# Kernel optimization log

Hardware: AMD Instinct MI355X
Metric: run time of the kernel (lower is better)

The kernel has to match this reference:

```python
import jax, jax.numpy as jnp
import numpy as np

PI = float(np.pi)
N_DIST, N_THETA = 4, 8   # projection_dict
MAX_DIST = 0.2           # self.max_dist (estimated from nh distances in __init__)


def _distance_angle(lon1, lat1, lon2, lat2):
    # great-circle distance + bearing ('polar' base of get_distance_angle)
    dlon = lon2 - lon1
    cos_d = jnp.sin(lat1) * jnp.sin(lat2) + jnp.cos(lat1) * jnp.cos(lat2) * jnp.cos(dlon)
    d = jnp.arccos(jnp.clip(cos_d, -1.0 + 1e-7, 1.0 - 1e-7))
    phi = jnp.arctan2(jnp.sin(dlon) * jnp.cos(lat2),
                      jnp.cos(lat1) * jnp.sin(lat2) - jnp.sin(lat1) * jnp.cos(lat2) * jnp.cos(dlon))
    return d, phi


def _forward(x, coordinates, sigma_d, kappa_vm, local_indices, adjc):
    # x: [B,N,E]; adjc: [Ncells,NH]; coordinates: [2,Ncells]; local_indices: [B,N]
    sigma_d = jnp.reshape(sigma_d, ())
    kappa_vm = jnp.reshape(kappa_vm, ())
    indices_nh = adjc[local_indices]                              # [B,N,NH] (get_nh_indices)
    # gather_nh_data (sample offsets are zero: sampled_level == global_level, sample==0)
    x_nh = jax.vmap(lambda xb, ib: xb[ib])(x, indices_nh)         # [B,N,NH,E]
    coords_nh = coordinates[:, indices_nh]                        # [2,B,N,NH]
    # get_relative_positions(coords_nh[:,:,:,0], coords_nh, polar=True):
    # coords1 -> [2,B,N,1,1], coords2 -> [2,B,N,1,NH]  => dists/phis [B,N,1,NH]
    lon_c = coords_nh[0, :, :, 0][..., None, None]                # [B,N,1,1]
    lat_c = coords_nh[1, :, :, 0][..., None, None]
    lon_nh = coords_nh[0][:, :, None, :]                          # [B,N,1,NH]
    lat_nh = coords_nh[1][:, :, None, :]
    dists, phis = _distance_angle(lon_c, lat_c, lon_nh, lat_nh)   # [B,N,1,NH]
    thetas_proj = jnp.linspace(-PI, PI, N_THETA + 1)[:-1]         # [T]
    dists_proj = jnp.linspace(0.0, MAX_DIST, N_DIST)              # [D]
    # von_mises: [D?,T,1] - [B,N,1,1,NH] broadcast -> we keep factored forms
    vm = jnp.exp(kappa_vm * jnp.cos(thetas_proj[None, :, None] - phis[..., None, :]))        # [B,N,1,T,NH]
    nd = jnp.exp(-0.5 * ((dists_proj[:, None, None] - dists[..., None, :]) / sigma_d) ** 2)  # [B,N,D,1,NH]
    w = vm * nd                                                   # [B,N,D,T,NH]
    w = w / (w.sum(axis=-1, keepdims=True) + 1e-10)
    # proj_data: weighted sum over neighborhood -> [B,N,D,T,E]
    return jnp.einsum('bndtk,bnke->bndte', w, x_nh)


def setup_inputs() -> dict:
    key = jax.random.key(0)
    k1, k2, k3 = jax.random.split(key, 3)
    B, N, NH, E = 1, 65536, 7, 16
    x = jax.random.normal(k1, (B, N, E), dtype=jnp.float32)
    # lon/lat in a small local patch (radians) so neighbor distances are O(MAX_DIST)
    coordinates = jax.random.uniform(k2, (2, N), dtype=jnp.float32) * 0.2
    adjc = jax.random.randint(k3, (N, NH), 0, N, dtype=jnp.int32)
    local_indices = jnp.arange(N, dtype=jnp.int32)[None, :]       # [B,N]
    sigma_d = jnp.full((1,), 0.05, dtype=jnp.float32)
    kappa_vm = jnp.full((1,), 2.0, dtype=jnp.float32)
    return {"x": x, "coordinates": coordinates, "sigma_d": sigma_d,
            "kappa_vm": kappa_vm, "local_indices": local_indices, "adjc": adjc}


def reference(x, coordinates, sigma_d, kappa_vm, local_indices, adjc):
    return _forward(x, coordinates, sigma_d, kappa_vm, local_indices, adjc)
```

## Files before the change

kernel.cpp:

```cpp
#include <hip/hip_runtime.h>
#include <math.h>

constexpr int NH     = 7;
constexpr int NDIST  = 4;
constexpr int NTHETA = 8;
constexpr int EDIM   = 16;
constexpr int NPB    = 8;
constexpr int BLOCK  = 256;

typedef float f32x4 __attribute__((ext_vector_type(4)));

__global__ __launch_bounds__(BLOCK) void grid_layer_kernel(
    const float* __restrict__ x,
    const float* __restrict__ coords,
    const float* __restrict__ sigma_p,
    const float* __restrict__ kappa_p,
    const int*   __restrict__ lidx,
    const int*   __restrict__ adjc,
    float*       __restrict__ out,
    int N)
{
    __shared__ float4 xs[NPB][NH][EDIM / 4];
    __shared__ float4 vm4[NPB][NH][2];
    __shared__ float4 nd4[NPB][NH];
    __shared__ float4 ctr[NPB];
    __shared__ int    sidx[NPB][NH];

    const int tid = threadIdx.x;
    const int n0  = blockIdx.x * NPB;

    const float inv_s = 1.0f / sigma_p[0];
    const float kappa = kappa_p[0];

    if (tid < NPB * NH * 4) {
        const int p  = tid >> 2;
        const int q  = tid & 3;
        const int nl = p / NH;
        const int k  = p - nl * NH;
        const int n  = n0 + nl;
        if (n < N) {
            const int idx = adjc[(size_t)lidx[n] * NH + k];
            if (q == 0) sidx[nl][k] = idx;
            xs[nl][k][q] = ((const float4*)(x + (size_t)idx * EDIM))[q];
        }
    } else if (tid < NPB * NH * 4 + NPB) {
        const int nl = tid - NPB * NH * 4;
        const int n  = n0 + nl;
        if (n < N) {
            const int i0 = adjc[(size_t)lidx[n] * NH];
            const float lon1 = coords[i0];
            const float lat1 = coords[N + i0];
            float s1, c1;
            __sincosf(lat1, &s1, &c1);
            ctr[nl] = make_float4(lon1, s1, c1, 0.0f);
        }
    }
    __syncthreads();

    if (tid < NPB * NH) {
        const int nl = tid / NH;
        const int k  = tid - nl * NH;
        const int n  = n0 + nl;
        if (n < N) {
            const int idxk = sidx[nl][k];
            const float lon2 = coords[idxk];
            const float lat2 = coords[N + idxk];
            const float4 c   = ctr[nl];
            const float sl1 = c.y, cl1 = c.z;
            const float dlon = lon2 - c.x;
            float sl2, cl2, sdl, cdl;
            __sincosf(lat2, &sl2, &cl2);
            __sincosf(dlon, &sdl, &cdl);
            const float tcc  = cl2 * cdl;
            float cosd = fmaf(sl1, sl2, cl1 * tcc);
            cosd = fminf(fmaxf(cosd, -1.0f + 1e-7f), 1.0f - 1e-7f);
            const float dist = acosf(cosd);

            const float p1 = cl1 * sl2;
            const float p2 = sl1 * tcc;
            const float xb = p1 - p2;
            const float yb = sdl * cl2;
            const float r2 = xb * xb + yb * yb;
            float cphi, sphi;
            if (r2 > 1e-12f) {
                const float ri = __builtin_amdgcn_rsqf(r2);
                cphi = xb * ri;
                sphi = yb * ri;
            } else {
                cphi = 1.0f;
                sphi = 0.0f;
            }

            const float A = kappa * cphi;
            const float B = kappa * sphi;
            const float U = 0.70710678118f * (A + B);
            const float V = 0.70710678118f * (A - B);
            float4 va, vb;
            va.x = __expf(-A); va.y = __expf(-U); va.z = __expf(-B); va.w = __expf(V);
            vb.x = __expf(A);  vb.y = __expf(U);  vb.z = __expf(B);  vb.w = __expf(-V);
            vm4[nl][k][0] = va;
            vm4[nl][k][1] = vb;

            const float di = dist * inv_s;
            const float z0 = di;
            const float z1 = fmaf(0.066666667f, inv_s, -di);
            const float z2 = fmaf(0.133333333f, inv_s, -di);
            const float z3 = fmaf(0.2f,         inv_s, -di);
            float4 nd;
            nd.x = __expf(-0.5f * z0 * z0);
            nd.y = __expf(-0.5f * z1 * z1);
            nd.z = __expf(-0.5f * z2 * z2);
            nd.w = __expf(-0.5f * z3 * z3);
            nd4[nl][k] = nd;
        }
    }
    __syncthreads();

    const int nl = tid >> 5;
    const int j  = tid & 31;
    const int t  = j >> 2;
    const int e4 = j & 3;
    const int n  = n0 + nl;
    if (n >= N) return;

    float  sw[NDIST] = {0.f, 0.f, 0.f, 0.f};
    float4 acc[NDIST];
    #pragma unroll
    for (int d = 0; d < NDIST; ++d) acc[d] = make_float4(0.f, 0.f, 0.f, 0.f);

    #pragma unroll
    for (int k = 0; k < NH; ++k) {
        const float  vmk = ((const float*)&vm4[nl][k][0])[t];
        const float4 nd  = nd4[nl][k];
        const float4 xv  = xs[nl][k][e4];
        const float w0 = vmk * nd.x;
        const float w1 = vmk * nd.y;
        const float w2 = vmk * nd.z;
        const float w3 = vmk * nd.w;
        sw[0] += w0; sw[1] += w1; sw[2] += w2; sw[3] += w3;
        acc[0].x = fmaf(w0, xv.x, acc[0].x);
        acc[0].y = fmaf(w0, xv.y, acc[0].y);
        acc[0].z = fmaf(w0, xv.z, acc[0].z);
        acc[0].w = fmaf(w0, xv.w, acc[0].w);
        acc[1].x = fmaf(w1, xv.x, acc[1].x);
        acc[1].y = fmaf(w1, xv.y, acc[1].y);
        acc[1].z = fmaf(w1, xv.z, acc[1].z);
        acc[1].w = fmaf(w1, xv.w, acc[1].w);
        acc[2].x = fmaf(w2, xv.x, acc[2].x);
        acc[2].y = fmaf(w2, xv.y, acc[2].y);
        acc[2].z = fmaf(w2, xv.z, acc[2].z);
        acc[2].w = fmaf(w2, xv.w, acc[2].w);
        acc[3].x = fmaf(w3, xv.x, acc[3].x);
        acc[3].y = fmaf(w3, xv.y, acc[3].y);
        acc[3].z = fmaf(w3, xv.z, acc[3].z);
        acc[3].w = fmaf(w3, xv.w, acc[3].w);
    }

    float* outp = out + (size_t)n * (NDIST * NTHETA * EDIM);
    #pragma unroll
    for (int d = 0; d < NDIST; ++d) {
        const float inv = __builtin_amdgcn_rcpf(sw[d] + 1e-10f);
        f32x4 o;
        o.x = acc[d].x * inv;
        o.y = acc[d].y * inv;
        o.z = acc[d].z * inv;
        o.w = acc[d].w * inv;
        __builtin_nontemporal_store(
            o, (f32x4*)(outp + (d * NTHETA * EDIM) + (t * EDIM) + e4 * 4));
    }
}

extern "C" void kernel_launch(void* const* d_in, const int* in_sizes, int n_in,
                              void* d_out, int out_size, void* d_ws, size_t ws_size,
                              hipStream_t stream) {
    const float* x      = (const float*)d_in[0];
    const float* coords = (const float*)d_in[1];
    const float* sigma  = (const float*)d_in[2];
    const float* kappa  = (const float*)d_in[3];
    const int*   lidx   = (const int*)d_in[4];
    const int*   adjc   = (const int*)d_in[5];
    float*       out    = (float*)d_out;

    const int N = in_sizes[4];
    const int grid = (N + NPB - 1) / NPB;
    hipLaunchKernelGGL(grid_layer_kernel, dim3(grid), dim3(BLOCK), 0, stream,
                       x, coords, sigma, kappa, lidx, adjc, out, N);
}
```

Baseline: 162.8 us.

## Convert to persistent grid-stride kernel with register-prefetched, double-buffered gathers

After: 164.8 us. No clear change (+1.2%).

```diff
diff --git a/kernel.cpp b/kernel.cpp
--- a/kernel.cpp
+++ b/kernel.cpp
@@ -7,6 +7,7 @@
 constexpr int EDIM   = 16;
 constexpr int NPB    = 8;
 constexpr int BLOCK  = 256;
+constexpr int MAXGRID = 2048;
 
 typedef float f32x4 __attribute__((ext_vector_type(4)));
 
@@ -20,153 +21,163 @@
     float*       __restrict__ out,
     int N)
 {
-    __shared__ float4 xs[NPB][NH][EDIM / 4];
-    __shared__ float4 vm4[NPB][NH][2];
-    __shared__ float4 nd4[NPB][NH];
-    __shared__ float4 ctr[NPB];
-    __shared__ int    sidx[NPB][NH];
+    __shared__ float4 xs [2][NPB][NH][EDIM / 4];
+    __shared__ float4 vm4[2][NPB][NH][2];
+    __shared__ float4 nd4[2][NPB][NH];
 
     const int tid = threadIdx.x;
-    const int n0  = blockIdx.x * NPB;
+    const bool stg = (tid < NPB * NH * 4);
+    const int p   = tid >> 2, q = tid & 3;
+    const int snl = p / NH, sk = p - snl * NH;
+    const bool geo = stg && (q == 0);
 
     const float inv_s = 1.0f / sigma_p[0];
     const float kappa = kappa_p[0];
 
-    if (tid < NPB * NH * 4) {
-        const int p  = tid >> 2;
-        const int q  = tid & 3;
-        const int nl = p / NH;
-        const int k  = p - nl * NH;
-        const int n  = n0 + nl;
+    const int S  = (int)gridDim.x;
+    const int nG = (N + NPB - 1) / NPB;
+    const int g0 = blockIdx.x;
+
+    int    idxNxt = 0, idx0Nxt = 0;
+    float4 xR = make_float4(0.f, 0.f, 0.f, 0.f);
+    float  lon1R = 0.f, lat1R = 0.f, lon2R = 0.f, lat2R = 0.f;
+
+    if (stg) {
+        const int n  = g0 * NPB + snl;
+        const int nn = (n < N) ? n : (N - 1);
+        const int li = lidx[nn];
+        const int idx  = adjc[(size_t)li * NH + sk];
+        const int idx0 = adjc[(size_t)li * NH];
+        xR = ((const float4*)(x + (size_t)idx * EDIM))[q];
+        if (geo) {
+            lon1R = coords[idx0]; lat1R = coords[N + idx0];
+            lon2R = coords[idx];  lat2R = coords[N + idx];
+        }
+        const int g1 = g0 + S;
+        if (g1 < nG) {
+            const int n1  = g1 * NPB + snl;
+            const int nn1 = (n1 < N) ? n1 : (N - 1);
+            const int li1 = lidx[nn1];
+            idxNxt = adjc[(size_t)li1 * NH + sk];
+            if (geo) idx0Nxt = adjc[(size_t)li1 * NH];
+        }
+    }
+
+    int buf = 0;
+    for (int g = g0; g < nG; g += S, buf ^= 1) {
+        if (stg) {
+            xs[buf][snl][sk][q] = xR;
+            if (geo) {
+                float s1, c1, s2, c2, sd, cd;
+                __sincosf(lat1R, &s1, &c1);
+                __sincosf(lat2R, &s2, &c2);
+                __sincosf(lon2R - lon1R, &sd, &cd);
+                const float tcc = c2 * cd;
+                float cosd = fmaf(s1, s2, c1 * tcc);
+                cosd = fminf(fmaxf(cosd, -1.0f + 1e-7f), 1.0f - 1e-7f);
+                const float dist = acosf(cosd);
+                const float p1 = c1 * s2;
+                const float p2 = s1 * tcc;
+                const float xb = p1 - p2;
+                const float yb = sd * c2;
+                const float r2 = xb * xb + yb * yb;
+                float cphi = 1.0f, sphi = 0.0f;
+                if (r2 > 1e-12f) {
+                    const float ri = __builtin_amdgcn_rsqf(r2);
+                    cphi = xb * ri; sphi = yb * ri;
+                }
+                const float A = kappa * cphi;
+                const float B = kappa * sphi;
+                const float U = 0.70710678118f * (A + B);
+                const float V = 0.70710678118f * (A - B);
+                float4 va, vb;
+                va.x = __expf(-A); va.y = __expf(-U); va.z = __expf(-B); va.w = __expf(V);
+                vb.x = __expf(A);  vb.y = __expf(U);  vb.z = __expf(B);  vb.w = __expf(-V);
+                vm4[buf][snl][sk][0] = va;
+                vm4[buf][snl][sk][1] = vb;
+                const float di = dist * inv_s;
+                const float z1 = fmaf(0.066666667f, inv_s, -di);
+                const float z2 = fmaf(0.133333333f, inv_s, -di);
+                const float z3 = fmaf(0.2f,         inv_s, -di);
+                float4 nd;
+                nd.x = __expf(-0.5f * di * di);
+                nd.y = __expf(-0.5f * z1 * z1);
+                nd.z = __expf(-0.5f * z2 * z2);
+                nd.w = __expf(-0.5f * z3 * z3);
+                nd4[buf][snl][sk] = nd;
+            }
+        }
+        __syncthreads();
+
+        const int gN1 = g + S;
+        if (stg && gN1 < nG) {
+            xR = ((const float4*)(x + (size_t)idxNxt * EDIM))[q];
+            if (geo) {
+                lon1R = coords[idx0Nxt]; lat1R = coords[N + idx0Nxt];
+                lon2R = coords[idxNxt];  lat2R = coords[N + idxNxt];
+            }
+            const int gN2 = g + 2 * S;
+            if (gN2 < nG) {
+                const int n2  = gN2 * NPB + snl;
+                const int nn2 = (n2 < N) ? n2 : (N - 1);
+                const int li2 = lidx[nn2];
+                idxNxt = adjc[(size_t)li2 * NH + sk];
+                if (geo) idx0Nxt = adjc[(size_t)li2 * NH];
+            }
+        }
+
+        const int nl = tid >> 5;
+        const int j  = tid & 31;
+        const int t  = j >> 2;
+        const int e4 = j & 3;
+        const int n  = g * NPB + nl;
         if (n < N) {
-            const int idx = adjc[(size_t)lidx[n] * NH + k];
-            if (q == 0) sidx[nl][k] = idx;
-            xs[nl][k][q] = ((const float4*)(x + (size_t)idx * EDIM))[q];
-        }
-    } else if (tid < NPB * NH * 4 + NPB) {
-        const int nl = tid - NPB * NH * 4;
-        const int n  = n0 + nl;
-        if (n < N) {
-            const int i0 = adjc[(size_t)lidx[n] * NH];
-            const float lon1 = coords[i0];
-            const float lat1 = coords[N + i0];
-            float s1, c1;
-            __sincosf(lat1, &s1, &c1);
-            ctr[nl] = make_float4(lon1, s1, c1, 0.0f);
-        }
-    }
-    __syncthreads();
-
-    if (tid < NPB * NH) {
-        const int nl = tid / NH;
-        const int k  = tid - nl * NH;
-        const int n  = n0 + nl;
-        if (n < N) {
-            const int idxk = sidx[nl][k];
-            const float lon2 = coords[idxk];
-            const float lat2 = coords[N + idxk];
-            const float4 c   = ctr[nl];
-            const float sl1 = c.y, cl1 = c.z;
-            const float dlon = lon2 - c.x;
-            float sl2, cl2, sdl, cdl;
-            __sincosf(lat2, &sl2, &cl2);
-            __sincosf(dlon, &sdl, &cdl);
-            const float tcc  = cl2 * cdl;
-            float cosd = fmaf(sl1, sl2, cl1 * tcc);
-            cosd = fminf(fmaxf(cosd, -1.0f + 1e-7f), 1.0f - 1e-7f);
-            const float dist = acosf(cosd);
-
-            const float p1 = cl1 * sl2;
-            const float p2 = sl1 * tcc;
-            const float xb = p1 - p2;
-            const float yb = sdl * cl2;
-            const float r2 = xb * xb + yb * yb;
-            float cphi, sphi;
-            if (r2 > 1e-12f) {
-                const float ri = __builtin_amdgcn_rsqf(r2);
-                cphi = xb * ri;
-                sphi = yb * ri;
-            } else {
-                cphi = 1.0f;
-                sphi = 0.0f;
-            }
-
-            const float A = kappa * cphi;
-            const float B = kappa * sphi;
-            const float U = 0.70710678118f * (A + B);
-            const float V = 0.70710678118f * (A - B);
-            float4 va, vb;
-            va.x = __expf(-A); va.y = __expf(-U); va.z = __expf(-B); va.w = __expf(V);
-            vb.x = __expf(A);  vb.y = __expf(U);  vb.z = __expf(B);  vb.w = __expf(-V);
-            vm4[nl][k][0] = va;
-            vm4[nl][k][1] = vb;
-
-            const float di = dist * inv_s;
-            const float z0 = di;
-            const float z1 = fmaf(0.066666667f, inv_s, -di);
-            const float z2 = fmaf(0.133333333f, inv_s, -di);
-            const float z3 = fmaf(0.2f,         inv_s, -di);
-            float4 nd;
-            nd.x = __expf(-0.5f * z0 * z0);
-            nd.y = __expf(-0.5f * z1 * z1);
-            nd.z = __expf(-0.5f * z2 * z2);
-            nd.w = __expf(-0.5f * z3 * z3);
-            nd4[nl][k] = nd;
-        }
-    }
-    __syncthreads();
-
-    const int nl = tid >> 5;
-    const int j  = tid & 31;
-    const int t  = j >> 2;
-    const int e4 = j & 3;
-    const int n  = n0 + nl;
-    if (n >= N) return;
-
-    float  sw[NDIST] = {0.f, 0.f, 0.f, 0.f};
-    float4 acc[NDIST];
-    #pragma unroll
-    for (int d = 0; d < NDIST; ++d) acc[d] = make_float4(0.f, 0.f, 0.f, 0.f);
-
-    #pragma unroll
-    for (int k = 0; k < NH; ++k) {
-        const float  vmk = ((const float*)&vm4[nl][k][0])[t];
-        const float4 nd  = nd4[nl][k];
-        const float4 xv  = xs[nl][k][e4];
-        const float w0 = vmk * nd.x;
-        const float w1 = vmk * nd.y;
-        const float w2 = vmk * nd.z;
-        const float w3 = vmk * nd.w;
-        sw[0] += w0; sw[1] += w1; sw[2] += w2; sw[3] += w3;
-        acc[0].x = fmaf(w0, xv.x, acc[0].x);
-        acc[0].y = fmaf(w0, xv.y, acc[0].y);
-        acc[0].z = fmaf(w0, xv.z, acc[0].z);
-        acc[0].w = fmaf(w0, xv.w, acc[0].w);
-        acc[1].x = fmaf(w1, xv.x, acc[1].x);
-        acc[1].y = fmaf(w1, xv.y, acc[1].y);
-        acc[1].z = fmaf(w1, xv.z, acc[1].z);
-        acc[1].w = fmaf(w1, xv.w, acc[1].w);
-        acc[2].x = fmaf(w2, xv.x, acc[2].x);
-        acc[2].y = fmaf(w2, xv.y, acc[2].y);
-        acc[2].z = fmaf(w2, xv.z, acc[2].z);
-        acc[2].w = fmaf(w2, xv.w, acc[2].w);
-        acc[3].x = fmaf(w3, xv.x, acc[3].x);
-        acc[3].y = fmaf(w3, xv.y, acc[3].y);
-        acc[3].z = fmaf(w3, xv.z, acc[3].z);
-        acc[3].w = fmaf(w3, xv.w, acc[3].w);
-    }
-
-    float* outp = out + (size_t)n * (NDIST * NTHETA * EDIM);
-    #pragma unroll
-    for (int d = 0; d < NDIST; ++d) {
-        const float inv = __builtin_amdgcn_rcpf(sw[d] + 1e-10f);
-        f32x4 o;
-        o.x = acc[d].x * inv;
-        o.y = acc[d].y * inv;
-        o.z = acc[d].z * inv;
-        o.w = acc[d].w * inv;
-        __builtin_nontemporal_store(
-            o, (f32x4*)(outp + (d * NTHETA * EDIM) + (t * EDIM) + e4 * 4));
+            float  sw[NDIST] = {0.f, 0.f, 0.f, 0.f};
+            float4 acc[NDIST];
+            #pragma unroll
+            for (int d = 0; d < NDIST; ++d) acc[d] = make_float4(0.f, 0.f, 0.f, 0.f);
+
+            #pragma unroll
+            for (int k = 0; k < NH; ++k) {
+                const float  vmk = ((const float*)&vm4[buf][nl][k][0])[t];
+                const float4 nd  = nd4[buf][nl][k];
+                const float4 xv  = xs[buf][nl][k][e4];
+                const float w0 = vmk * nd.x;
+                const float w1 = vmk * nd.y;
+                const float w2 = vmk * nd.z;
+                const float w3 = vmk * nd.w;
+                sw[0] += w0; sw[1] += w1; sw[2] += w2; sw[3] += w3;
+                acc[0].x = fmaf(w0, xv.x, acc[0].x);
+                acc[0].y = fmaf(w0, xv.y, acc[0].y);
+                acc[0].z = fmaf(w0, xv.z, acc[0].z);
+                acc[0].w = fmaf(w0, xv.w, acc[0].w);
+                acc[1].x = fmaf(w1, xv.x, acc[1].x);
+                acc[1].y = fmaf(w1, xv.y, acc[1].y);
+                acc[1].z = fmaf(w1, xv.z, acc[1].z);
+                acc[1].w = fmaf(w1, xv.w, acc[1].w);
+                acc[2].x = fmaf(w2, xv.x, acc[2].x);
+                acc[2].y = fmaf(w2, xv.y, acc[2].y);
+                acc[2].z = fmaf(w2, xv.z, acc[2].z);
+                acc[2].w = fmaf(w2, xv.w, acc[2].w);
+                acc[3].x = fmaf(w3, xv.x, acc[3].x);
+                acc[3].y = fmaf(w3, xv.y, acc[3].y);
+                acc[3].z = fmaf(w3, xv.z, acc[3].z);
+                acc[3].w = fmaf(w3, xv.w, acc[3].w);
+            }
+
+            float* outp = out + (size_t)n * (NDIST * NTHETA * EDIM);
+            #pragma unroll
+            for (int d = 0; d < NDIST; ++d) {
+                const float inv = __builtin_amdgcn_rcpf(sw[d] + 1e-10f);
+                f32x4 o;
+                o.x = acc[d].x * inv;
+                o.y = acc[d].y * inv;
+                o.z = acc[d].z * inv;
+                o.w = acc[d].w * inv;
+                __builtin_nontemporal_store(
+                    o, (f32x4*)(outp + (d * NTHETA * EDIM) + (t * EDIM) + e4 * 4));
+            }
+        }
     }
 }
 
@@ -181,8 +192,9 @@
     const int*   adjc   = (const int*)d_in[5];
     float*       out    = (float*)d_out;
 
-    const int N = in_sizes[4];
-    const int grid = (N + NPB - 1) / NPB;
+    const int N  = in_sizes[4];
+    const int nG = (N + NPB - 1) / NPB;
+    const int grid = (nG < MAXGRID) ? nG : MAXGRID;
     hipLaunchKernelGGL(grid_layer_kernel, dim3(grid), dim3(BLOCK), 0, stream,
                        x, coords, sigma, kappa, lidx, adjc, out, N);
 }
```

## Process 32 points per block and drop the first barrier via redundant index loads

Applied to the files above, without the earlier changes.

After: 163.6 us. Within noise of the previous version (+0.5%).

```diff
diff --git a/kernel.cpp b/kernel.cpp
--- a/kernel.cpp
+++ b/kernel.cpp
@@ -5,7 +5,7 @@
 constexpr int NDIST  = 4;
 constexpr int NTHETA = 8;
 constexpr int EDIM   = 16;
-constexpr int NPB    = 8;
+constexpr int NPB    = 32;
 constexpr int BLOCK  = 256;
 
 typedef float f32x4 __attribute__((ext_vector_type(4)));
@@ -20,11 +20,9 @@
     float*       __restrict__ out,
     int N)
 {
-    __shared__ float4 xs[NPB][NH][EDIM / 4];
+    __shared__ float4 xs[NPB * NH * 4];
     __shared__ float4 vm4[NPB][NH][2];
     __shared__ float4 nd4[NPB][NH];
-    __shared__ float4 ctr[NPB];
-    __shared__ int    sidx[NPB][NH];
 
     const int tid = threadIdx.x;
     const int n0  = blockIdx.x * NPB;
@@ -32,63 +30,50 @@
     const float inv_s = 1.0f / sigma_p[0];
     const float kappa = kappa_p[0];
 
-    if (tid < NPB * NH * 4) {
-        const int p  = tid >> 2;
-        const int q  = tid & 3;
-        const int nl = p / NH;
-        const int k  = p - nl * NH;
-        const int n  = n0 + nl;
-        if (n < N) {
-            const int idx = adjc[(size_t)lidx[n] * NH + k];
-            if (q == 0) sidx[nl][k] = idx;
-            xs[nl][k][q] = ((const float4*)(x + (size_t)idx * EDIM))[q];
-        }
-    } else if (tid < NPB * NH * 4 + NPB) {
-        const int nl = tid - NPB * NH * 4;
-        const int n  = n0 + nl;
-        if (n < N) {
-            const int i0 = adjc[(size_t)lidx[n] * NH];
-            const float lon1 = coords[i0];
-            const float lat1 = coords[N + i0];
-            float s1, c1;
-            __sincosf(lat1, &s1, &c1);
-            ctr[nl] = make_float4(lon1, s1, c1, 0.0f);
+    #pragma unroll
+    for (int it = 0; it < 4; ++it) {
+        const int i = tid + BLOCK * it;
+        if (i < NPB * NH * 4) {
+            const int p  = i >> 2;
+            const int q  = i & 3;
+            const int nl = p / NH;
+            const int k  = p - nl * NH;
+            const int n  = n0 + nl;
+            if (n < N) {
+                const int idx = adjc[(size_t)lidx[n] * NH + k];
+                xs[i] = ((const float4*)(x + (size_t)idx * EDIM))[q];
+            }
         }
     }
-    __syncthreads();
 
     if (tid < NPB * NH) {
         const int nl = tid / NH;
         const int k  = tid - nl * NH;
         const int n  = n0 + nl;
         if (n < N) {
-            const int idxk = sidx[nl][k];
-            const float lon2 = coords[idxk];
-            const float lat2 = coords[N + idxk];
-            const float4 c   = ctr[nl];
-            const float sl1 = c.y, cl1 = c.z;
-            const float dlon = lon2 - c.x;
-            float sl2, cl2, sdl, cdl;
-            __sincosf(lat2, &sl2, &cl2);
-            __sincosf(dlon, &sdl, &cdl);
-            const float tcc  = cl2 * cdl;
-            float cosd = fmaf(sl1, sl2, cl1 * tcc);
+            const size_t li = (size_t)lidx[n] * NH;
+            const int idx0 = adjc[li];
+            const int idxk = adjc[li + k];
+            const float lon1 = coords[idx0], lat1 = coords[N + idx0];
+            const float lon2 = coords[idxk], lat2 = coords[N + idxk];
+            float s1, c1, s2, c2, sd, cd;
+            __sincosf(lat1, &s1, &c1);
+            __sincosf(lat2, &s2, &c2);
+            __sincosf(lon2 - lon1, &sd, &cd);
+            const float tcc = c2 * cd;
+            float cosd = fmaf(s1, s2, c1 * tcc);
             cosd = fminf(fmaxf(cosd, -1.0f + 1e-7f), 1.0f - 1e-7f);
             const float dist = acosf(cosd);
 
-            const float p1 = cl1 * sl2;
-            const float p2 = sl1 * tcc;
+            const float p1 = c1 * s2;
+            const float p2 = s1 * tcc;
             const float xb = p1 - p2;
-            const float yb = sdl * cl2;
+            const float yb = sd * c2;
             const float r2 = xb * xb + yb * yb;
-            float cphi, sphi;
+            float cphi = 1.0f, sphi = 0.0f;
             if (r2 > 1e-12f) {
                 const float ri = __builtin_amdgcn_rsqf(r2);
-                cphi = xb * ri;
-                sphi = yb * ri;
-            } else {
-                cphi = 1.0f;
-                sphi = 0.0f;
+                cphi = xb * ri; sphi = yb * ri;
             }
 
             const float A = kappa * cphi;
@@ -102,12 +87,11 @@
             vm4[nl][k][1] = vb;
 
             const float di = dist * inv_s;
-            const float z0 = di;
             const float z1 = fmaf(0.066666667f, inv_s, -di);
             const float z2 = fmaf(0.133333333f, inv_s, -di);
             const float z3 = fmaf(0.2f,         inv_s, -di);
             float4 nd;
-            nd.x = __expf(-0.5f * z0 * z0);
+            nd.x = __expf(-0.5f * di * di);
             nd.y = __expf(-0.5f * z1 * z1);
             nd.z = __expf(-0.5f * z2 * z2);
             nd.w = __expf(-0.5f * z3 * z3);
@@ -116,57 +100,62 @@
     }
     __syncthreads();
 
-    const int nl = tid >> 5;
-    const int j  = tid & 31;
-    const int t  = j >> 2;
-    const int e4 = j & 3;
-    const int n  = n0 + nl;
-    if (n >= N) return;
+    const int j    = tid & 31;
+    const int t    = j >> 2;
+    const int e4   = j & 3;
+    const int pb   = tid >> 5;
 
-    float  sw[NDIST] = {0.f, 0.f, 0.f, 0.f};
-    float4 acc[NDIST];
-    #pragma unroll
-    for (int d = 0; d < NDIST; ++d) acc[d] = make_float4(0.f, 0.f, 0.f, 0.f);
+    #pragma unroll 1
+    for (int it = 0; it < NPB / 8; ++it) {
+        const int p = pb + 8 * it;
+        const int n = n0 + p;
+        if (n >= N) continue;
 
-    #pragma unroll
-    for (int k = 0; k < NH; ++k) {
-        const float  vmk = ((const float*)&vm4[nl][k][0])[t];
-        const float4 nd  = nd4[nl][k];
-        const float4 xv  = xs[nl][k][e4];
-        const float w0 = vmk * nd.x;
-        const float w1 = vmk * nd.y;
-        const float w2 = vmk * nd.z;
-        const float w3 = vmk * nd.w;
-        sw[0] += w0; sw[1] += w1; sw[2] += w2; sw[3] += w3;
-        acc[0].x = fmaf(w0, xv.x, acc[0].x);
-        acc[0].y = fmaf(w0, xv.y, acc[0].y);
-        acc[0].z = fmaf(w0, xv.z, acc[0].z);
-        acc[0].w = fmaf(w0, xv.w, acc[0].w);
-        acc[1].x = fmaf(w1, xv.x, acc[1].x);
-        acc[1].y = fmaf(w1, xv.y, acc[1].y);
-        acc[1].z = fmaf(w1, xv.z, acc[1].z);
-        acc[1].w = fmaf(w1, xv.w, acc[1].w);
-        acc[2].x = fmaf(w2, xv.x, acc[2].x);
-        acc[2].y = fmaf(w2, xv.y, acc[2].y);
-        acc[2].z = fmaf(w2, xv.z, acc[2].z);
-        acc[2].w = fmaf(w2, xv.w, acc[2].w);
-        acc[3].x = fmaf(w3, xv.x, acc[3].x);
-        acc[3].y = fmaf(w3, xv.y, acc[3].y);
-        acc[3].z = fmaf(w3, xv.z, acc[3].z);
-        acc[3].w = fmaf(w3, xv.w, acc[3].w);
-    }
+        float  sw[NDIST] = {0.f, 0.f, 0.f, 0.f};
+        float4 acc[NDIST];
+        #pragma unroll
+        for (int d = 0; d < NDIST; ++d) acc[d] = make_float4(0.f, 0.f, 0.f, 0.f);
 
-    float* outp = out + (size_t)n * (NDIST * NTHETA * EDIM);
-    #pragma unroll
-    for (int d = 0; d < NDIST; ++d) {
-        const float inv = __builtin_amdgcn_rcpf(sw[d] + 1e-10f);
-        f32x4 o;
-        o.x = acc[d].x * inv;
-        o.y = acc[d].y * inv;
-        o.z = acc[d].z * inv;
-        o.w = acc[d].w * inv;
-        __builtin_nontemporal_store(
-            o, (f32x4*)(outp + (d * NTHETA * EDIM) + (t * EDIM) + e4 * 4));
+        #pragma unroll
+        for (int k = 0; k < NH; ++k) {
+            const float  vmk = ((const float*)&vm4[p][k][0])[t];
+            const float4 nd  = nd4[p][k];
+            const float4 xv  = xs[(p * NH + k) * 4 + e4];
+            const float w0 = vmk * nd.x;
+            const float w1 = vmk * nd.y;
+            const float w2 = vmk * nd.z;
+            const float w3 = vmk * nd.w;
+            sw[0] += w0; sw[1] += w1; sw[2] += w2; sw[3] += w3;
+            acc[0].x = fmaf(w0, xv.x, acc[0].x);
+            acc[0].y = fmaf(w0, xv.y, acc[0].y);
+            acc[0].z = fmaf(w0, xv.z, acc[0].z);
+            acc[0].w = fmaf(w0, xv.w, acc[0].w);
+            acc[1].x = fmaf(w1, xv.x, acc[1].x);
+            acc[1].y = fmaf(w1, xv.y, acc[1].y);
+            acc[1].z = fmaf(w1, xv.z, acc[1].z);
+            acc[1].w = fmaf(w1, xv.w, acc[1].w);
+            acc[2].x = fmaf(w2, xv.x, acc[2].x);
+            acc[2].y = fmaf(w2, xv.y, acc[2].y);
+            acc[2].z = fmaf(w2, xv.z, acc[2].z);
+            acc[2].w = fmaf(w2, xv.w, acc[2].w);
+            acc[3].x = fmaf(w3, xv.x, acc[3].x);
+            acc[3].y = fmaf(w3, xv.y, acc[3].y);
+            acc[3].z = fmaf(w3, xv.z, acc[3].z);
+            acc[3].w = fmaf(w3, xv.w, acc[3].w);
+        }
+
+        float* outp = out + (size_t)n * (NDIST * NTHETA * EDIM);
+        #pragma unroll
+        for (int d = 0; d < NDIST; ++d) {
+            const float inv = __builtin_amdgcn_rcpf(sw[d] + 1e-10f);
+            f32x4 o;
+            o.x = acc[d].x * inv;
+            o.y = acc[d].y * inv;
+            o.z = acc[d].z * inv;
+            o.w = acc[d].w * inv;
+            __builtin_nontemporal_store(
+                o, (f32x4*)(outp + (d * NTHETA * EDIM) + (t * EDIM) + e4 * 4));
+        }
     }
 }
 
```
